# Performance work log

Hardware: AMD Instinct MI355X
Metric: run time of the kernel (lower is better)

The kernel has to match this reference:

```python
import jax, jax.numpy as jnp
import numpy as np

ATOM = 34
HID = 256
LATENT = 128
CELLS = 512
B, N = 64, 128
NEG = -9e15


def setup_inputs() -> dict:
    key = jax.random.key(0)
    ks = jax.random.split(key, 20)
    inp = {}
    inp["xs"] = jax.random.normal(ks[0], (B, N, ATOM), dtype=jnp.float32)
    inp["A"] = jax.random.randint(ks[1], (B, N, N), 0, 2, dtype=jnp.int32)
    inp["cell_emb"] = jax.random.normal(ks[2], (B, CELLS), dtype=jnp.float32)
    inp["Wg"] = jax.random.normal(ks[3], (3, ATOM, ATOM), dtype=jnp.float32) * 0.17
    inp["bg"] = jnp.zeros((3, ATOM), dtype=jnp.float32)
    inp["attn"] = jax.random.normal(ks[4], (3, 2 * ATOM), dtype=jnp.float32) * 0.17
    # W_gnn_trans: 34 -> 256
    inp["Wt"] = jax.random.normal(ks[5], (ATOM, HID), dtype=jnp.float32) * 0.08
    inp["bt"] = jnp.zeros((HID,), dtype=jnp.float32)
    # ffn: 256 -> 34 ; ffn2: 34 -> latent
    inp["Wf"] = jax.random.normal(ks[6], (HID, ATOM), dtype=jnp.float32) * 0.08
    inp["bf"] = jnp.zeros((ATOM,), dtype=jnp.float32)
    inp["Wf2"] = jax.random.normal(ks[7], (ATOM, LATENT), dtype=jnp.float32) * 0.11
    inp["bf2"] = jnp.zeros((LATENT,), dtype=jnp.float32)
    # Decoder MLP: (latent+cells)->128->256->512->1
    din = LATENT + CELLS
    inp["W1"] = jax.random.normal(ks[8], (din, 128), dtype=jnp.float32) * 0.05
    inp["b1"] = jnp.zeros((128,), dtype=jnp.float32)
    inp["W2"] = jax.random.normal(ks[9], (128, 256), dtype=jnp.float32) * 0.07
    inp["b2"] = jnp.zeros((256,), dtype=jnp.float32)
    inp["W3"] = jax.random.normal(ks[10], (256, 512), dtype=jnp.float32) * 0.05
    inp["b3"] = jnp.zeros((512,), dtype=jnp.float32)
    inp["W4"] = jax.random.normal(ks[11], (512, 1), dtype=jnp.float32) * 0.06
    inp["b4"] = jnp.zeros((1,), dtype=jnp.float32)
    return inp


def reference(xs, A, cell_emb, Wg, bg, attn, Wt, bt, Wf, bf, Wf2, bf2,
              W1, b1, W2, b2, W3, b3, W4, b4):
    # ---- gnn(): 3 rounds of GAT-style masked-softmax message passing ----
    # a_input[b,p,q] = [h[b,p], h[b,q]], so e = leaky_relu(h@a1 outer+ h@a2)
    h0 = xs
    mask = A > 0  # [B,N,N]
    x = xs
    for i in range(3):
        h = jax.nn.relu(jnp.einsum('bnd,de->bne', x, Wg[i]) + bg[i])  # [B,N,34]
        f_src = h @ attn[i, :ATOM]   # [B,N] -- score contribution of row atom
        f_dst = h @ attn[i, ATOM:]   # [B,N] -- score contribution of col atom
        e = jax.nn.leaky_relu(f_src[:, :, None] + f_dst[:, None, :], 0.01)
        scores = jnp.where(mask, e, NEG)
        att = jax.nn.softmax(scores, axis=2)  # dropout disabled (deterministic)
        x = x + jnp.einsum('bpq,bqd->bpd', att, h)
    g = jax.nn.relu(jnp.einsum('bnd,dh->bnh', x, Wt) + bt)  # [B,N,HID]

    # ---- VEC_forward ----
    d = jnp.einsum('bnh,hd->bnd', g, Wf) + bf + h0        # ffn + residual to input xs
    d = jnp.einsum('bnd,dl->bnl', d, Wf2) + bf2           # [B,N,LATENT]
    d = jnp.max(d, axis=1)                                # [B,LATENT]
    vec = jax.nn.sigmoid(jnp.concatenate([d, cell_emb], axis=-1))

    # ---- Decoder_mlp (dropout disabled) ----
    hminus = jax.nn.relu(vec @ W1 + b1)
    hminus = jax.nn.relu(hminus @ W2 + b2)
    hminus = jax.nn.relu(hminus @ W3 + b3)
    score = hminus @ W4 + b4                              # [B,1]
    return score
```

## Files before the change

kernel.cpp:

```cpp
#include <hip/hip_runtime.h>

constexpr int ATOM = 34;
constexpr int HID = 256;
constexpr int LATENT = 128;
constexpr int CELLS = 512;
constexpr int NN = 128;
constexpr int NA = NN * ATOM;
#define NEGF (-9e15f)

__global__ __launch_bounds__(512) void k_gat(
    const float* __restrict__ xsrc, const int* __restrict__ A,
    const float* __restrict__ Wg, const float* __restrict__ bg,
    const float* __restrict__ av, float* __restrict__ X)
{
    const int b = blockIdx.x >> 2, qq = blockIdx.x & 3;
    const int t = threadIdx.x, lane = t & 63, wave = t >> 6;
    const int p0 = qq * 32;

    __shared__ float xl[NN][ATOM + 1];
    __shared__ float hl[NN][ATOM + 1];
    __shared__ float att[32][NN];
    __shared__ float fs[NN], fd[NN];
    __shared__ float wg[ATOM * ATOM];
    __shared__ float bgs[ATOM], avs[2 * ATOM];

    for (int i = t; i < ATOM * ATOM; i += 512) wg[i] = Wg[i];
    if (t < ATOM)     bgs[t] = bg[t];
    if (t < 2 * ATOM) avs[t] = av[t];
    const float* xp = xsrc + b * NA;
    for (int i = t; i < NA; i += 512) xl[i / ATOM][i % ATOM] = xp[i];
    __syncthreads();

    for (int i = t; i < NA; i += 512) {
        int n = i / ATOM, e = i % ATOM;
        float acc = bgs[e];
        #pragma unroll
        for (int d = 0; d < ATOM; ++d) acc += xl[n][d] * wg[d * ATOM + e];
        hl[n][e] = fmaxf(acc, 0.f);
    }
    __syncthreads();

    if (t < 2 * NN) {
        int n = t & (NN - 1), w = t >> 7;
        float acc = 0.f;
        #pragma unroll
        for (int d = 0; d < ATOM; ++d) acc += hl[n][d] * avs[w * ATOM + d];
        if (w == 0) fs[n] = acc; else fd[n] = acc;
    }
    __syncthreads();

    const int* Ab = A + b * NN * NN;
    #pragma unroll
    for (int i = 0; i < 4; ++i) {
        int lp = wave * 4 + i, gp = p0 + lp;
        float fsv = fs[gp];
        unsigned long long m0 = __ballot(Ab[gp * NN + lane] > 0);
        unsigned long long m1 = __ballot(Ab[gp * NN + 64 + lane] > 0);
        float s0 = fsv + fd[lane];
        s0 = (s0 > 0.f) ? s0 : 0.01f * s0;
        if (!((m0 >> lane) & 1ull)) s0 = NEGF;
        float s1 = fsv + fd[64 + lane];
        s1 = (s1 > 0.f) ? s1 : 0.01f * s1;
        if (!((m1 >> lane) & 1ull)) s1 = NEGF;
        float mx = fmaxf(s0, s1);
        #pragma unroll
        for (int o = 32; o >= 1; o >>= 1) mx = fmaxf(mx, __shfl_xor(mx, o, 64));
        float e0 = __expf(s0 - mx), e1 = __expf(s1 - mx);
        float sm = e0 + e1;
        #pragma unroll
        for (int o = 32; o >= 1; o >>= 1) sm += __shfl_xor(sm, o, 64);
        float inv = 1.f / sm;
        att[lp][lane]      = e0 * inv;
        att[lp][64 + lane] = e1 * inv;
    }
    __syncthreads();

    for (int i = t; i < 32 * ATOM; i += 512) {
        int lp = i / ATOM, d = i % ATOM, gp = p0 + lp;
        float acc = xl[gp][d];
        #pragma unroll 4
        for (int q = 0; q < NN; ++q) acc += att[lp][q] * hl[q][d];
        X[b * NA + gp * ATOM + d] = acc;
    }
}

__global__ __launch_bounds__(512) void k_phaseB(
    const float* __restrict__ X, const float* __restrict__ xs,
    const float* __restrict__ Wt, const float* __restrict__ bt,
    const float* __restrict__ Wf, const float* __restrict__ bf,
    const float* __restrict__ Wf2, const float* __restrict__ bf2,
    float* __restrict__ DM)
{
    const int b = blockIdx.x >> 2, qq = blockIdx.x & 3;
    const int t = threadIdx.x;
    const int p0 = qq * 32;
    __shared__ float wt[HID * (ATOM + 1)];
    __shared__ float wf[HID * (ATOM + 1)];
    __shared__ float bts[HID];
    __shared__ float bfs[ATOM];
    __shared__ float xl[32][ATOM + 1];
    __shared__ float dl[32][ATOM + 1];
    __shared__ float sl[512];

    for (int i = t; i < ATOM * HID; i += 512) { int d = i / HID, h = i % HID; wt[h * 35 + d] = Wt[i]; }
    for (int i = t; i < HID * ATOM; i += 512) { int h = i / ATOM, j = i % ATOM; wf[h * 35 + j] = Wf[i]; }
    if (t < HID) bts[t] = bt[t];
    if (t < ATOM) bfs[t] = bf[t];
    for (int i = t; i < 32 * ATOM; i += 512) xl[i / ATOM][i % ATOM] = X[b * NA + p0 * ATOM + i];
    __syncthreads();

    const int row = t & 31, sub = t >> 5;
    float xr[ATOM];
    #pragma unroll
    for (int d = 0; d < ATOM; ++d) xr[d] = xl[row][d];
    float dp[ATOM];
    #pragma unroll
    for (int j = 0; j < ATOM; ++j) dp[j] = 0.f;
    #pragma unroll 2
    for (int i = 0; i < 16; ++i) {
        const int h = sub + 16 * i;
        float acc = bts[h];
        #pragma unroll
        for (int d = 0; d < ATOM; ++d) acc += xr[d] * wt[h * 35 + d];
        acc = fmaxf(acc, 0.f);
        #pragma unroll
        for (int j = 0; j < ATOM; ++j) dp[j] += acc * wf[h * 35 + j];
    }
    __syncthreads();
    float* pl = (sub < 8) ? wt : wf;
    #pragma unroll
    for (int j = 0; j < ATOM; ++j) pl[((sub & 7) * 32 + row) * ATOM + j] = dp[j];
    __syncthreads();
    for (int i = t; i < 32 * ATOM; i += 512) {
        int rr = i / ATOM, j = i % ATOM;
        float dv = bfs[j] + xs[b * NA + (p0 + rr) * ATOM + j];
        #pragma unroll
        for (int s = 0; s < 8; ++s)
            dv += wt[(s * 32 + rr) * ATOM + j] + wf[(s * 32 + rr) * ATOM + j];
        dl[rr][j] = dv;
    }
    __syncthreads();
    const int l = t & 127, chunk = t >> 7;
    float mx = -3.4e38f;
    for (int rr = chunk * 8; rr < chunk * 8 + 8; ++rr) {
        float acc = bf2[l];
        #pragma unroll
        for (int j = 0; j < ATOM; ++j) acc += dl[rr][j] * Wf2[j * LATENT + l];
        mx = fmaxf(mx, acc);
    }
    sl[chunk * 128 + l] = mx;
    __syncthreads();
    if (t < LATENT)
        DM[(b * 4 + qq) * LATENT + t] =
            fmaxf(fmaxf(sl[t], sl[128 + t]), fmaxf(sl[256 + t], sl[384 + t]));
}

__global__ __launch_bounds__(256) void k_dec1(
    const float* __restrict__ DM, const float* __restrict__ cell,
    const float* __restrict__ W1, const float* __restrict__ b1,
    float* __restrict__ H1)
{
    const int b = blockIdx.x, t = threadIdx.x;
    __shared__ float vec[LATENT + CELLS];
    __shared__ float sl[256];
    if (t < LATENT) {
        float m = fmaxf(fmaxf(DM[(b * 4 + 0) * LATENT + t], DM[(b * 4 + 1) * LATENT + t]),
                        fmaxf(DM[(b * 4 + 2) * LATENT + t], DM[(b * 4 + 3) * LATENT + t]));
        vec[t] = 1.f / (1.f + __expf(-m));
    }
    vec[LATENT + t]       = 1.f / (1.f + __expf(-cell[b * CELLS + t]));
    vec[LATENT + 256 + t] = 1.f / (1.f + __expf(-cell[b * CELLS + 256 + t]));
    __syncthreads();
    const int j = t & 127, half = t >> 7;
    float acc = 0.f;
    for (int k = half * 320; k < half * 320 + 320; ++k)
        acc += vec[k] * W1[k * 128 + j];
    sl[half * 128 + j] = acc;
    __syncthreads();
    if (t < 128)
        H1[b * 128 + t] = fmaxf(sl[t] + sl[128 + t] + b1[t], 0.f);
}

__global__ __launch_bounds__(512) void k_dec2(
    const float* __restrict__ H1,
    const float* __restrict__ W2, const float* __restrict__ b2,
    const float* __restrict__ W3, const float* __restrict__ b3,
    const float* __restrict__ W4, const float* __restrict__ b4,
    float* __restrict__ out)
{
    const int b = blockIdx.x, t = threadIdx.x, lane = t & 63, wave = t >> 6;
    __shared__ float h1[128], h2[256], h3[512], sl[512];
    if (t < 128) h1[t] = H1[b * 128 + t];
    __syncthreads();
    {
        const int j = t & 255, half = t >> 8;
        float acc = 0.f;
        #pragma unroll 4
        for (int k = half * 64; k < half * 64 + 64; ++k)
            acc += h1[k] * W2[k * 256 + j];
        sl[half * 256 + j] = acc;
    }
    __syncthreads();
    if (t < 256) h2[t] = fmaxf(sl[t] + sl[256 + t] + b2[t], 0.f);
    __syncthreads();
    {
        float acc = b3[t];
        #pragma unroll 4
        for (int k = 0; k < 256; ++k) acc += h2[k] * W3[k * 512 + t];
        h3[t] = fmaxf(acc, 0.f);
    }
    __syncthreads();
    float v = h3[t] * W4[t];
    #pragma unroll
    for (int o = 32; o >= 1; o >>= 1) v += __shfl_xor(v, o, 64);
    if (lane == 0) sl[wave] = v;
    __syncthreads();
    if (t == 0) {
        float s = b4[0];
        #pragma unroll
        for (int w = 0; w < 8; ++w) s += sl[w];
        out[b] = s;
    }
}

extern "C" void kernel_launch(void* const* d_in, const int* in_sizes, int n_in,
                              void* d_out, int out_size, void* d_ws, size_t ws_size,
                              hipStream_t stream) {
    const float* xs       = (const float*)d_in[0];
    const int*   A        = (const int*)  d_in[1];
    const float* cell_emb = (const float*)d_in[2];
    const float* Wg       = (const float*)d_in[3];
    const float* bg       = (const float*)d_in[4];
    const float* attnv    = (const float*)d_in[5];
    const float* Wt       = (const float*)d_in[6];
    const float* bt       = (const float*)d_in[7];
    const float* Wf       = (const float*)d_in[8];
    const float* bf       = (const float*)d_in[9];
    const float* Wf2      = (const float*)d_in[10];
    const float* bf2      = (const float*)d_in[11];
    const float* W1       = (const float*)d_in[12];
    const float* b1       = (const float*)d_in[13];
    const float* W2       = (const float*)d_in[14];
    const float* b2       = (const float*)d_in[15];
    const float* W3       = (const float*)d_in[16];
    const float* b3       = (const float*)d_in[17];
    const float* W4       = (const float*)d_in[18];
    const float* b4       = (const float*)d_in[19];
    float* out = (float*)d_out;

    float* W  = (float*)d_ws;
    float* Xb = W;
    float* DM = W + 278528;
    float* H1 = W + 311296;

    for (int r = 0; r < 3; ++r) {
        const float* xsrc = (r == 0) ? xs : Xb;
        k_gat<<<256, 512, 0, stream>>>(xsrc, A, Wg + r * ATOM * ATOM, bg + r * ATOM,
                                       attnv + r * 2 * ATOM, Xb);
    }
    k_phaseB<<<256, 512, 0, stream>>>(Xb, xs, Wt, bt, Wf, bf, Wf2, bf2, DM);
    k_dec1<<<64, 256, 0, stream>>>(DM, cell_emb, W1, b1, H1);
    k_dec2<<<64, 512, 0, stream>>>(H1, W2, b2, W3, b3, W4, b4, out);
}
```

Measured before the change: 209.2 us.

## Vectorize GAT/phaseB smem layouts, ping-pong GAT buffers, fuse decoder kernels

Transposes h in shared memory and pads rows to 36 so the H computation, the attention aggregation and the phaseB MLP can use float4 shared-memory loads. Wf2 is staged in shared memory and held in registers. The two decoder kernels are merged into a single 1024-thread kernel that splits the K dimension more finely, removing one launch and the H1 round trip. The GAT rounds now alternate between two buffers, which avoids in-place read/write hazards across blocks of the same batch.

```diff
diff --git a/kernel.cpp b/kernel.cpp
--- a/kernel.cpp
+++ b/kernel.cpp
@@ -13,15 +13,15 @@
     const float* __restrict__ Wg, const float* __restrict__ bg,
     const float* __restrict__ av, float* __restrict__ X)
 {
-    const int b = blockIdx.x >> 2, qq = blockIdx.x & 3;
+    const int b = blockIdx.x >> 2, q4 = blockIdx.x & 3;
     const int t = threadIdx.x, lane = t & 63, wave = t >> 6;
-    const int p0 = qq * 32;
-
-    __shared__ float xl[NN][ATOM + 1];
-    __shared__ float hl[NN][ATOM + 1];
+    const int p0 = q4 * 32;
+
+    __shared__ float xl[NN][36];
+    __shared__ float hlT[ATOM][132];
     __shared__ float att[32][NN];
+    __shared__ float wg[ATOM * ATOM];
     __shared__ float fs[NN], fd[NN];
-    __shared__ float wg[ATOM * ATOM];
     __shared__ float bgs[ATOM], avs[2 * ATOM];
 
     for (int i = t; i < ATOM * ATOM; i += 512) wg[i] = Wg[i];
@@ -31,20 +31,28 @@
     for (int i = t; i < NA; i += 512) xl[i / ATOM][i % ATOM] = xp[i];
     __syncthreads();
 
-    for (int i = t; i < NA; i += 512) {
-        int n = i / ATOM, e = i % ATOM;
-        float acc = bgs[e];
-        #pragma unroll
-        for (int d = 0; d < ATOM; ++d) acc += xl[n][d] * wg[d * ATOM + e];
-        hl[n][e] = fmaxf(acc, 0.f);
+    {
+        const int n = t >> 2, sub = t & 3;
+        float xr[36];
+        float4* xr4 = (float4*)xr;
+        const float4* xlr = (const float4*)&xl[n][0];
+        #pragma unroll
+        for (int k = 0; k < 9; ++k) xr4[k] = xlr[k];
+        for (int e = sub; e < ATOM; e += 4) {
+            float acc = bgs[e];
+            #pragma unroll
+            for (int d = 0; d < ATOM; ++d) acc += xr[d] * wg[d * ATOM + e];
+            hlT[e][n] = fmaxf(acc, 0.f);
+        }
     }
     __syncthreads();
 
     if (t < 2 * NN) {
-        int n = t & (NN - 1), w = t >> 7;
+        const int n = t & (NN - 1), w = t >> 7;
+        const float* avp = avs + w * ATOM;
         float acc = 0.f;
         #pragma unroll
-        for (int d = 0; d < ATOM; ++d) acc += hl[n][d] * avs[w * ATOM + d];
+        for (int d = 0; d < ATOM; ++d) acc += hlT[d][n] * avp[d];
         if (w == 0) fs[n] = acc; else fd[n] = acc;
     }
     __syncthreads();
@@ -75,12 +83,32 @@
     }
     __syncthreads();
 
-    for (int i = t; i < 32 * ATOM; i += 512) {
-        int lp = i / ATOM, d = i % ATOM, gp = p0 + lp;
-        float acc = xl[gp][d];
-        #pragma unroll 4
-        for (int q = 0; q < NN; ++q) acc += att[lp][q] * hl[q][d];
-        X[b * NA + gp * ATOM + d] = acc;
+    {
+        const int p = t >> 4, g = t & 15;
+        const float4* ap  = (const float4*)&att[p][0];
+        const float4* h1p = (const float4*)&hlT[g][0];
+        const float4* h2p = (const float4*)&hlT[g + 16][0];
+        float a1 = 0.f, a2 = 0.f;
+        #pragma unroll 8
+        for (int k = 0; k < 32; ++k) {
+            float4 a4 = ap[k], x1 = h1p[k], x2 = h2p[k];
+            a1 += a4.x * x1.x + a4.y * x1.y + a4.z * x1.z + a4.w * x1.w;
+            a2 += a4.x * x2.x + a4.y * x2.y + a4.z * x2.z + a4.w * x2.w;
+        }
+        const int gp = p0 + p;
+        float* Xr = X + b * NA + gp * ATOM;
+        Xr[g]      = xl[gp][g] + a1;
+        Xr[g + 16] = xl[gp][g + 16] + a2;
+        if (g < 2) {
+            const float4* h3p = (const float4*)&hlT[g + 32][0];
+            float a3 = 0.f;
+            #pragma unroll 8
+            for (int k = 0; k < 32; ++k) {
+                float4 a4 = ap[k], x3 = h3p[k];
+                a3 += a4.x * x3.x + a4.y * x3.y + a4.z * x3.z + a4.w * x3.w;
+            }
+            Xr[g + 32] = xl[gp][g + 32] + a3;
+        }
     }
 }
 
@@ -91,45 +119,71 @@
     const float* __restrict__ Wf2, const float* __restrict__ bf2,
     float* __restrict__ DM)
 {
-    const int b = blockIdx.x >> 2, qq = blockIdx.x & 3;
+    const int b = blockIdx.x >> 2, q4 = blockIdx.x & 3;
     const int t = threadIdx.x;
-    const int p0 = qq * 32;
-    __shared__ float wt[HID * (ATOM + 1)];
-    __shared__ float wf[HID * (ATOM + 1)];
+    const int p0 = q4 * 32;
+    __shared__ float wt[HID * 36];
+    __shared__ float wf[HID * 36];
+    __shared__ float xl[32][36];
+    __shared__ float dlT[ATOM][33];
+    __shared__ float wf2s[ATOM * LATENT];
     __shared__ float bts[HID];
     __shared__ float bfs[ATOM];
-    __shared__ float xl[32][ATOM + 1];
-    __shared__ float dl[32][ATOM + 1];
     __shared__ float sl[512];
 
-    for (int i = t; i < ATOM * HID; i += 512) { int d = i / HID, h = i % HID; wt[h * 35 + d] = Wt[i]; }
-    for (int i = t; i < HID * ATOM; i += 512) { int h = i / ATOM, j = i % ATOM; wf[h * 35 + j] = Wf[i]; }
-    if (t < HID) bts[t] = bt[t];
+    for (int i = t; i < ATOM * HID; i += 512) {
+        int d = i >> 8, h = i & 255;
+        wt[h * 36 + d] = Wt[i];
+    }
+    for (int i = t; i < HID * ATOM; i += 512) {
+        int h = i / ATOM, j = i % ATOM;
+        wf[h * 36 + j] = Wf[i];
+    }
+    for (int i = t; i < ATOM * LATENT; i += 512) wf2s[i] = Wf2[i];
+    if (t < HID)  bts[t] = bt[t];
     if (t < ATOM) bfs[t] = bf[t];
     for (int i = t; i < 32 * ATOM; i += 512) xl[i / ATOM][i % ATOM] = X[b * NA + p0 * ATOM + i];
     __syncthreads();
 
     const int row = t & 31, sub = t >> 5;
-    float xr[ATOM];
-    #pragma unroll
-    for (int d = 0; d < ATOM; ++d) xr[d] = xl[row][d];
     float dp[ATOM];
     #pragma unroll
     for (int j = 0; j < ATOM; ++j) dp[j] = 0.f;
-    #pragma unroll 2
-    for (int i = 0; i < 16; ++i) {
-        const int h = sub + 16 * i;
-        float acc = bts[h];
-        #pragma unroll
-        for (int d = 0; d < ATOM; ++d) acc += xr[d] * wt[h * 35 + d];
-        acc = fmaxf(acc, 0.f);
-        #pragma unroll
-        for (int j = 0; j < ATOM; ++j) dp[j] += acc * wf[h * 35 + j];
-    }
-    __syncthreads();
-    float* pl = (sub < 8) ? wt : wf;
-    #pragma unroll
-    for (int j = 0; j < ATOM; ++j) pl[((sub & 7) * 32 + row) * ATOM + j] = dp[j];
+    {
+        float xr[36];
+        float4* xr4 = (float4*)xr;
+        const float4* xlr = (const float4*)&xl[row][0];
+        #pragma unroll
+        for (int k = 0; k < 9; ++k) xr4[k] = xlr[k];
+        for (int i = 0; i < 16; ++i) {
+            const int h = sub + 16 * i;
+            float acc = bts[h];
+            const float4* wtp = (const float4*)&wt[h * 36];
+            #pragma unroll
+            for (int k = 0; k < 8; ++k) {
+                float4 w4 = wtp[k];
+                acc += xr[4*k] * w4.x + xr[4*k+1] * w4.y + xr[4*k+2] * w4.z + xr[4*k+3] * w4.w;
+            }
+            acc += xr[32] * wt[h * 36 + 32] + xr[33] * wt[h * 36 + 33];
+            acc = fmaxf(acc, 0.f);
+            const float4* wfp = (const float4*)&wf[h * 36];
+            #pragma unroll
+            for (int k = 0; k < 8; ++k) {
+                float4 w4 = wfp[k];
+                dp[4*k]   += acc * w4.x; dp[4*k+1] += acc * w4.y;
+                dp[4*k+2] += acc * w4.z; dp[4*k+3] += acc * w4.w;
+            }
+            dp[32] += acc * wf[h * 36 + 32];
+            dp[33] += acc * wf[h * 36 + 33];
+        }
+    }
+    __syncthreads();
+    {
+        float* pl = (sub < 8) ? wt : wf;
+        const int s8 = sub & 7;
+        #pragma unroll
+        for (int j = 0; j < ATOM; ++j) pl[(s8 * 32 + row) * ATOM + j] = dp[j];
+    }
     __syncthreads();
     for (int i = t; i < 32 * ATOM; i += 512) {
         int rr = i / ATOM, j = i % ATOM;
@@ -137,80 +191,89 @@
         #pragma unroll
         for (int s = 0; s < 8; ++s)
             dv += wt[(s * 32 + rr) * ATOM + j] + wf[(s * 32 + rr) * ATOM + j];
-        dl[rr][j] = dv;
-    }
-    __syncthreads();
-    const int l = t & 127, chunk = t >> 7;
-    float mx = -3.4e38f;
-    for (int rr = chunk * 8; rr < chunk * 8 + 8; ++rr) {
-        float acc = bf2[l];
-        #pragma unroll
-        for (int j = 0; j < ATOM; ++j) acc += dl[rr][j] * Wf2[j * LATENT + l];
-        mx = fmaxf(mx, acc);
-    }
-    sl[chunk * 128 + l] = mx;
+        dlT[j][rr] = dv;
+    }
+    __syncthreads();
+    {
+        const int l = t & 127, chunk = t >> 7;
+        float w2r[ATOM];
+        #pragma unroll
+        for (int j = 0; j < ATOM; ++j) w2r[j] = wf2s[j * LATENT + l];
+        float mx = -3.4e38f;
+        for (int rr = chunk * 8; rr < chunk * 8 + 8; ++rr) {
+            float acc = bf2[l];
+            #pragma unroll
+            for (int j = 0; j < ATOM; ++j) acc += dlT[j][rr] * w2r[j];
+            mx = fmaxf(mx, acc);
+        }
+        sl[chunk * 128 + l] = mx;
+    }
     __syncthreads();
     if (t < LATENT)
-        DM[(b * 4 + qq) * LATENT + t] =
+        DM[(b * 4 + q4) * LATENT + t] =
             fmaxf(fmaxf(sl[t], sl[128 + t]), fmaxf(sl[256 + t], sl[384 + t]));
 }
 
-__global__ __launch_bounds__(256) void k_dec1(
+__global__ __launch_bounds__(1024) void k_dec(
     const float* __restrict__ DM, const float* __restrict__ cell,
     const float* __restrict__ W1, const float* __restrict__ b1,
-    float* __restrict__ H1)
-{
-    const int b = blockIdx.x, t = threadIdx.x;
-    __shared__ float vec[LATENT + CELLS];
-    __shared__ float sl[256];
-    if (t < LATENT) {
-        float m = fmaxf(fmaxf(DM[(b * 4 + 0) * LATENT + t], DM[(b * 4 + 1) * LATENT + t]),
-                        fmaxf(DM[(b * 4 + 2) * LATENT + t], DM[(b * 4 + 3) * LATENT + t]));
-        vec[t] = 1.f / (1.f + __expf(-m));
-    }
-    vec[LATENT + t]       = 1.f / (1.f + __expf(-cell[b * CELLS + t]));
-    vec[LATENT + 256 + t] = 1.f / (1.f + __expf(-cell[b * CELLS + 256 + t]));
-    __syncthreads();
-    const int j = t & 127, half = t >> 7;
-    float acc = 0.f;
-    for (int k = half * 320; k < half * 320 + 320; ++k)
-        acc += vec[k] * W1[k * 128 + j];
-    sl[half * 128 + j] = acc;
-    __syncthreads();
-    if (t < 128)
-        H1[b * 128 + t] = fmaxf(sl[t] + sl[128 + t] + b1[t], 0.f);
-}
-
-__global__ __launch_bounds__(512) void k_dec2(
-    const float* __restrict__ H1,
     const float* __restrict__ W2, const float* __restrict__ b2,
     const float* __restrict__ W3, const float* __restrict__ b3,
     const float* __restrict__ W4, const float* __restrict__ b4,
     float* __restrict__ out)
 {
     const int b = blockIdx.x, t = threadIdx.x, lane = t & 63, wave = t >> 6;
-    __shared__ float h1[128], h2[256], h3[512], sl[512];
-    if (t < 128) h1[t] = H1[b * 128 + t];
-    __syncthreads();
-    {
-        const int j = t & 255, half = t >> 8;
+    __shared__ float vec[LATENT + CELLS];
+    __shared__ float h1[128], h2[256], h3[512];
+    __shared__ float sl[1024];
+    if (t < LATENT) {
+        float m = fmaxf(fmaxf(DM[(b*4+0)*LATENT + t], DM[(b*4+1)*LATENT + t]),
+                        fmaxf(DM[(b*4+2)*LATENT + t], DM[(b*4+3)*LATENT + t]));
+        vec[t] = 1.f / (1.f + __expf(-m));
+    } else if (t >= 512) {
+        int c = t - 512;
+        vec[LATENT + c] = 1.f / (1.f + __expf(-cell[b * CELLS + c]));
+    }
+    __syncthreads();
+    {
+        const int j = t & 127, part = t >> 7;
         float acc = 0.f;
         #pragma unroll 4
-        for (int k = half * 64; k < half * 64 + 64; ++k)
+        for (int k = part * 80; k < part * 80 + 80; ++k)
+            acc += vec[k] * W1[k * 128 + j];
+        sl[part * 128 + j] = acc;
+    }
+    __syncthreads();
+    if (t < 128) {
+        float v = b1[t];
+        #pragma unroll
+        for (int p = 0; p < 8; ++p) v += sl[p * 128 + t];
+        h1[t] = fmaxf(v, 0.f);
+    }
+    __syncthreads();
+    {
+        const int j = t & 255, part = t >> 8;
+        float acc = 0.f;
+        #pragma unroll 4
+        for (int k = part * 32; k < part * 32 + 32; ++k)
             acc += h1[k] * W2[k * 256 + j];
-        sl[half * 256 + j] = acc;
-    }
-    __syncthreads();
-    if (t < 256) h2[t] = fmaxf(sl[t] + sl[256 + t] + b2[t], 0.f);
-    __syncthreads();
-    {
-        float acc = b3[t];
+        sl[part * 256 + j] = acc;
+    }
+    __syncthreads();
+    if (t < 256) h2[t] = fmaxf(sl[t] + sl[256 + t] + sl[512 + t] + sl[768 + t] + b2[t], 0.f);
+    __syncthreads();
+    {
+        const int j = t & 511, part = t >> 9;
+        float acc = 0.f;
         #pragma unroll 4
-        for (int k = 0; k < 256; ++k) acc += h2[k] * W3[k * 512 + t];
-        h3[t] = fmaxf(acc, 0.f);
-    }
-    __syncthreads();
-    float v = h3[t] * W4[t];
+        for (int k = part * 128; k < part * 128 + 128; ++k)
+            acc += h2[k] * W3[k * 512 + j];
+        sl[part * 512 + j] = acc;
+    }
+    __syncthreads();
+    if (t < 512) h3[t] = fmaxf(sl[t] + sl[512 + t] + b3[t], 0.f);
+    __syncthreads();
+    float v = (t < 512) ? h3[t] * W4[t] : 0.f;
     #pragma unroll
     for (int o = 32; o >= 1; o >>= 1) v += __shfl_xor(v, o, 64);
     if (lane == 0) sl[wave] = v;
@@ -218,7 +281,7 @@
     if (t == 0) {
         float s = b4[0];
         #pragma unroll
-        for (int w = 0; w < 8; ++w) s += sl[w];
+        for (int w = 0; w < 16; ++w) s += sl[w];
         out[b] = s;
     }
 }
@@ -249,16 +312,13 @@
     float* out = (float*)d_out;
 
     float* W  = (float*)d_ws;
-    float* Xb = W;
-    float* DM = W + 278528;
-    float* H1 = W + 311296;
-
-    for (int r = 0; r < 3; ++r) {
-        const float* xsrc = (r == 0) ? xs : Xb;
-        k_gat<<<256, 512, 0, stream>>>(xsrc, A, Wg + r * ATOM * ATOM, bg + r * ATOM,
-                                       attnv + r * 2 * ATOM, Xb);
-    }
-    k_phaseB<<<256, 512, 0, stream>>>(Xb, xs, Wt, bt, Wf, bf, Wf2, bf2, DM);
-    k_dec1<<<64, 256, 0, stream>>>(DM, cell_emb, W1, b1, H1);
-    k_dec2<<<64, 512, 0, stream>>>(H1, W2, b2, W3, b3, W4, b4, out);
+    float* X0 = W;
+    float* X1 = W + 278528;
+    float* DM = W + 557056;
+
+    k_gat<<<256, 512, 0, stream>>>(xs, A, Wg,                  bg,          attnv,          X0);
+    k_gat<<<256, 512, 0, stream>>>(X0, A, Wg + ATOM * ATOM,    bg + ATOM,   attnv + 2*ATOM, X1);
+    k_gat<<<256, 512, 0, stream>>>(X1, A, Wg + 2 * ATOM * ATOM, bg + 2*ATOM, attnv + 4*ATOM, X0);
+    k_phaseB<<<256, 512, 0, stream>>>(X0, xs, Wt, bt, Wf, bf, Wf2, bf2, DM);
+    k_dec<<<64, 1024, 0, stream>>>(DM, cell_emb, W1, b1, W2, b2, W3, b3, W4, b4, out);
 }
```

Result: faster. 178.6 us (-14.6%).
